# Kernel tuning notes

Measured on AMD Instinct MI355X. Metric: run time of the kernel, lower is better.

The kernel has to match this reference:

```python
import jax, jax.numpy as jnp
import numpy as np

N, E = 50000, 800000
IN_DIM, HID, OUT_DIM = 512, 64, 40


def setup_inputs() -> dict:
    key = jax.random.key(0)
    ks = jax.random.split(key, 7)
    X = jax.random.normal(ks[0], (N, IN_DIM), dtype=jnp.float32)
    edges = jax.random.randint(ks[1], (2, E), 0, N, dtype=jnp.int64)
    # GCNConv weight (glorot) and bias
    W1 = jax.random.normal(ks[2], (IN_DIM, HID), dtype=jnp.float32) / np.sqrt(IN_DIM)
    b1 = jnp.zeros((HID,), dtype=jnp.float32)
    # fc Linear
    Wfc = jax.random.normal(ks[3], (OUT_DIM, HID), dtype=jnp.float32) / np.sqrt(HID)
    bfc = jax.random.normal(ks[4], (OUT_DIM,), dtype=jnp.float32) * 0.01
    return {"X": X, "edges": edges, "W1": W1, "b1": b1, "Wfc": Wfc, "bfc": bfc}


def gcn_conv(x, src, dst, W, b, n):
    # PyG GCNConv: transform, add self-loops, symmetric D^-1/2 A D^-1/2 norm,
    # scatter-add messages at destination, add bias.
    h = x @ W  # [N, HID]
    loop = jnp.arange(n, dtype=src.dtype)
    src = jnp.concatenate([src, loop])
    dst = jnp.concatenate([dst, loop])
    deg = jax.ops.segment_sum(jnp.ones_like(dst, dtype=h.dtype), dst, num_segments=n)
    dinv = jnp.where(deg > 0, jax.lax.rsqrt(deg), 0.0)
    coef = dinv[src] * dinv[dst]  # [E+N]
    msgs = coef[:, None] * h[src]  # gather + scale
    agg = jax.ops.segment_sum(msgs, dst, num_segments=n)  # scatter-add
    return agg + b


def reference(X, edges, W1, b1, Wfc, bfc):
    n = X.shape[0]
    src, dst = edges[0], edges[1]
    h = jax.nn.relu(gcn_conv(X, src, dst, W1, b1, n))  # [N, HID]
    return h @ Wfc.T + bfc  # [N, OUT_DIM]
```

## Files before the change

kernel.cpp:

```cpp
#include <hip/hip_runtime.h>
#include <hip/hip_bf16.h>

typedef unsigned short u16;
typedef __bf16 bf16_8 __attribute__((ext_vector_type(8)));
typedef float f32_4 __attribute__((ext_vector_type(4)));

#define IN_DIM 512
#define HID 64
#define OUT_DIM 40
#define CAP 64
#define CF_GRID 2048

__global__ void k_prep(const float* __restrict__ W1, u16* __restrict__ W1t,
                       int* __restrict__ cnt, int n) {
    int i = blockIdx.x * 256 + threadIdx.x;
    if (i < n) cnt[i] = 0;
    if (i < IN_DIM * HID) {
        int k = i / HID, o = i % HID;
        __hip_bfloat16 v = __float2bfloat16(W1[i]);
        W1t[o * IN_DIM + k] = *reinterpret_cast<u16*>(&v);
    }
}

__launch_bounds__(256)
__global__ void k_cf(const int* __restrict__ src, const int* __restrict__ dst,
                     int* cnt, u16* __restrict__ csr, int E) {
    int e = blockIdx.x * 256 + threadIdx.x;
    const int stride = CF_GRID * 256;
    for (; e < E; e += stride) {
        int d = dst[e];
        int p = atomicAdd(&cnt[d], 1);
        if (p < CAP) csr[(size_t)d * CAP + p] = (u16)src[e];
    }
}

__launch_bounds__(512)
__global__ void k_gemm(const float* __restrict__ X, const u16* __restrict__ W1t,
                       u16* __restrict__ hs, int N) {
    __shared__ __align__(16) u16 As[2][2][64 * 40];
    __shared__ __align__(16) float Red[64 * 64];
    const int t = threadIdx.x;
    const int g = t >> 8;
    const int wl = (t >> 6) & 3;
    const int lane = t & 63;
    const int m = lane & 15;
    const int quad = lane >> 4;
    const int n0 = blockIdx.x * 64;

    f32_4 acc[4];
    #pragma unroll
    for (int c = 0; c < 4; c++) acc[c] = (f32_4){0.f, 0.f, 0.f, 0.f};

    const int tg = t & 255;
    const int r_st = tg >> 2;
    const int k_st = (tg & 3) * 8;

    int row = n0 + r_st; if (row >= N) row = N - 1;
    const float* xp = X + (size_t)row * IN_DIM + g * 256 + k_st;

    f32_4 x0 = *reinterpret_cast<const f32_4*>(xp);
    f32_4 x1 = *reinterpret_cast<const f32_4*>(xp + 4);

    int buf = 0;
    for (int ks = 0; ks < 256; ks += 32) {
        u16 xb[8];
        #pragma unroll
        for (int q = 0; q < 4; q++) {
            __hip_bfloat16 c0 = __float2bfloat16(x0[q]);
            __hip_bfloat16 c1 = __float2bfloat16(x1[q]);
            xb[q]     = *reinterpret_cast<u16*>(&c0);
            xb[4 + q] = *reinterpret_cast<u16*>(&c1);
        }
        *reinterpret_cast<uint4*>(&As[g][buf][r_st * 40 + k_st]) = *reinterpret_cast<uint4*>(xb);
        __syncthreads();

        if (ks + 32 < 256) {
            x0 = *reinterpret_cast<const f32_4*>(xp + ks + 32);
            x1 = *reinterpret_cast<const f32_4*>(xp + ks + 36);
        }

        bf16_8 a = *reinterpret_cast<const bf16_8*>(&As[g][buf][(wl * 16 + m) * 40 + quad * 8]);
        #pragma unroll
        for (int c = 0; c < 4; c++) {
            bf16_8 b = *reinterpret_cast<const bf16_8*>(
                W1t + (size_t)(c * 16 + m) * IN_DIM + g * 256 + ks + quad * 8);
            acc[c] = __builtin_amdgcn_mfma_f32_16x16x32_bf16(a, b, acc[c], 0, 0, 0);
        }
        buf ^= 1;
    }

    if (g == 1) {
        #pragma unroll
        for (int r = 0; r < 4; r++)
            #pragma unroll
            for (int c = 0; c < 4; c++)
                Red[(wl * 16 + quad * 4 + r) * 64 + c * 16 + m] = acc[c][r];
    }
    __syncthreads();
    if (g == 0) {
        const int nbase = n0 + wl * 16 + quad * 4;
        #pragma unroll
        for (int r = 0; r < 4; r++) {
            int n = nbase + r;
            if (n < N) {
                #pragma unroll
                for (int c = 0; c < 4; c++) {
                    float s = acc[c][r] + Red[(wl * 16 + quad * 4 + r) * 64 + c * 16 + m];
                    __hip_bfloat16 hv = __float2bfloat16(s);
                    hs[(size_t)n * HID + c * 16 + m] = *reinterpret_cast<u16*>(&hv);
                }
            }
        }
    }
}

__global__ void k_scale(u16* __restrict__ hs, const int* __restrict__ cnt, int N) {
    int i = blockIdx.x * 256 + threadIdx.x;
    int node = i >> 3;
    if (node >= N) return;
    float dv = rsqrtf((float)cnt[node] + 1.0f);
    uint4 v = *reinterpret_cast<uint4*>(hs + (size_t)i * 8);
    uint vv[4] = {v.x, v.y, v.z, v.w};
    u16 o[8];
    #pragma unroll
    for (int q = 0; q < 4; q++) {
        float lo = __uint_as_float(vv[q] << 16) * dv;
        float hi = __uint_as_float(vv[q] & 0xFFFF0000u) * dv;
        __hip_bfloat16 bl_ = __float2bfloat16(lo);
        __hip_bfloat16 bh_ = __float2bfloat16(hi);
        o[2 * q]     = *reinterpret_cast<u16*>(&bl_);
        o[2 * q + 1] = *reinterpret_cast<u16*>(&bh_);
    }
    *reinterpret_cast<uint4*>(hs + (size_t)i * 8) = *reinterpret_cast<uint4*>(o);
}

__device__ __forceinline__ void acc_add(f32_4& a, uint2 v) {
    a[0] += __uint_as_float(v.x << 16);
    a[1] += __uint_as_float(v.x & 0xFFFF0000u);
    a[2] += __uint_as_float(v.y << 16);
    a[3] += __uint_as_float(v.y & 0xFFFF0000u);
}

#define SHP 72

__launch_bounds__(256)
__global__ void k_aggfc(const u16* __restrict__ hs, const u16* __restrict__ csr,
                        const int* __restrict__ cnt, const float* __restrict__ b1,
                        const float* __restrict__ Wfc, const float* __restrict__ bfc,
                        float* __restrict__ out, int N) {
    __shared__ __align__(16) u16 shb[16 * SHP];
    __shared__ __align__(16) u16 wfb[48 * SHP];
    __shared__ float bl[48];
    const int t = threadIdx.x;

    for (int i = t; i < 48 * HID; i += 256) {
        int o = i / HID, k = i % HID;
        float v = (o < OUT_DIM) ? Wfc[o * HID + k] : 0.f;
        __hip_bfloat16 b = __float2bfloat16(v);
        wfb[o * SHP + k] = *reinterpret_cast<u16*>(&b);
    }
    if (t < 48) bl[t] = (t < OUT_DIM) ? bfc[t] : 0.f;

    const int g = t >> 4, l = t & 15;
    const int n = blockIdx.x * 16 + g;

    if (n < N) {
        const uint2* hs2 = reinterpret_cast<const uint2*>(hs);
        f32_4 aa[4];
        #pragma unroll
        for (int q = 0; q < 4; q++) aa[q] = (f32_4){0.f, 0.f, 0.f, 0.f};
        const float dvn = rsqrtf((float)cnt[n] + 1.0f);
        acc_add(aa[0], hs2[(size_t)n * 16 + l]);
        int deg = cnt[n]; if (deg > CAP) deg = CAP;
        uint2 cv = reinterpret_cast<const uint2*>(csr + (size_t)n * CAP)[l];
        const int nn1 = N - 1;
        for (int j = 0; j < deg; j += 16) {
            int base = j >> 2;
            uint wx[4], wy[4];
            #pragma unroll
            for (int q = 0; q < 4; q++) {
                wx[q] = __shfl(cv.x, base + q, 16);
                wy[q] = __shfl(cv.y, base + q, 16);
            }
            int s[16];
            #pragma unroll
            for (int q = 0; q < 4; q++) {
                s[4 * q + 0] = (int)(wx[q] & 0xffff);
                s[4 * q + 1] = (int)(wx[q] >> 16);
                s[4 * q + 2] = (int)(wy[q] & 0xffff);
                s[4 * q + 3] = (int)(wy[q] >> 16);
            }
            uint2 v[16];
            #pragma unroll
            for (int i = 0; i < 16; i++) {
                int si = s[i] < nn1 ? s[i] : nn1;
                v[i] = hs2[(size_t)si * 16 + l];
            }
            #pragma unroll
            for (int i = 0; i < 16; i++) {
                if (j + i >= deg) { v[i].x = 0u; v[i].y = 0u; }
                acc_add(aa[i & 3], v[i]);
            }
        }
        f32_4 acc = (aa[0] + aa[1]) + (aa[2] + aa[3]);
        u16 rb[4];
        #pragma unroll
        for (int q = 0; q < 4; q++) {
            float x = dvn * acc[q] + b1[l * 4 + q];
            x = x > 0.f ? x : 0.f;
            __hip_bfloat16 hb = __float2bfloat16(x);
            rb[q] = *reinterpret_cast<u16*>(&hb);
        }
        *reinterpret_cast<uint2*>(&shb[g * SHP + l * 4]) = *reinterpret_cast<uint2*>(rb);
    }
    __syncthreads();

    const int wave = t >> 6;
    const int lane = t & 63;
    const int m = lane & 15;
    const int quad = lane >> 4;
    if (wave < 3) {
        bf16_8 a0 = *reinterpret_cast<const bf16_8*>(&shb[m * SHP + quad * 8]);
        bf16_8 a1 = *reinterpret_cast<const bf16_8*>(&shb[m * SHP + 32 + quad * 8]);
        bf16_8 b0 = *reinterpret_cast<const bf16_8*>(&wfb[(wave * 16 + m) * SHP + quad * 8]);
        bf16_8 b1 = *reinterpret_cast<const bf16_8*>(&wfb[(wave * 16 + m) * SHP + 32 + quad * 8]);
        f32_4 c = (f32_4){0.f, 0.f, 0.f, 0.f};
        c = __builtin_amdgcn_mfma_f32_16x16x32_bf16(a0, b0, c, 0, 0, 0);
        c = __builtin_amdgcn_mfma_f32_16x16x32_bf16(a1, b1, c, 0, 0, 0);
        const int o = wave * 16 + m;
        if (o < OUT_DIM) {
            const int base = blockIdx.x * 16;
            #pragma unroll
            for (int r = 0; r < 4; r++) {
                int node = base + quad * 4 + r;
                if (node < N) out[(size_t)node * OUT_DIM + o] = c[r] + bl[o];
            }
        }
    }
}


extern "C" void kernel_launch(void* const* d_in, const int* in_sizes, int n_in,
                              void* d_out, int out_size, void* d_ws, size_t ws_size,
                              hipStream_t stream) {
    const float* X   = (const float*)d_in[0];
    const int* edges = (const int*)d_in[1];
    const float* W1  = (const float*)d_in[2];
    const float* b1  = (const float*)d_in[3];
    const float* Wfc = (const float*)d_in[4];
    const float* bfc = (const float*)d_in[5];

    const int N = in_sizes[0] / IN_DIM;
    const int E = in_sizes[1] / 2;
    const int* src = edges;
    const int* dst = edges + E;

    char* p = (char*)d_ws;
    auto carve = [&](size_t bytes) -> char* {
        char* r = p;
        p += (bytes + 255) & ~(size_t)255;
        return r;
    };
    u16* W1t = (u16*)carve((size_t)IN_DIM * HID * 2);
    u16* hs  = (u16*)carve((size_t)N * HID * 2);
    int* cnt = (int*)carve((size_t)N * 4);
    u16* csr = (u16*)carve((size_t)N * CAP * 2);

    const int nb = (N + 255) / 256;
    const int NT = (N + 63) / 64;

    k_prep <<<nb, 256, 0, stream>>>(W1, W1t, cnt, N);
    k_cf   <<<CF_GRID, 256, 0, stream>>>(src, dst, cnt, csr, E);
    k_gemm <<<NT, 512, 0, stream>>>(X, W1t, hs, N);
    k_scale<<<(N * 8 + 255) / 256, 256, 0, stream>>>(hs, cnt, N);
    k_aggfc<<<(N + 15) / 16, 256, 0, stream>>>(hs, csr, cnt, b1, Wfc, bfc,
                                               (float*)d_out, N);
}
```

Baseline: 259.2 us.

## Merge edge CSR build into GEMM kernel as extra blocks to overlap

```diff
diff --git a/kernel.cpp b/kernel.cpp
--- a/kernel.cpp
+++ b/kernel.cpp
@@ -9,7 +9,7 @@
 #define HID 64
 #define OUT_DIM 40
 #define CAP 64
-#define CF_GRID 2048
+#define CF_BLK 256
 
 __global__ void k_prep(const float* __restrict__ W1, u16* __restrict__ W1t,
                        int* __restrict__ cnt, int n) {
@@ -22,30 +22,40 @@
     }
 }
 
-__launch_bounds__(256)
-__global__ void k_cf(const int* __restrict__ src, const int* __restrict__ dst,
-                     int* cnt, u16* __restrict__ csr, int E) {
-    int e = blockIdx.x * 256 + threadIdx.x;
-    const int stride = CF_GRID * 256;
-    for (; e < E; e += stride) {
-        int d = dst[e];
-        int p = atomicAdd(&cnt[d], 1);
-        if (p < CAP) csr[(size_t)d * CAP + p] = (u16)src[e];
-    }
-}
-
 __launch_bounds__(512)
-__global__ void k_gemm(const float* __restrict__ X, const u16* __restrict__ W1t,
-                       u16* __restrict__ hs, int N) {
+__global__ void k_work(const float* __restrict__ X, const u16* __restrict__ W1t,
+                       const int* __restrict__ src, const int* __restrict__ dst,
+                       int* cnt, u16* __restrict__ csr, u16* __restrict__ hs,
+                       int N, int E) {
     __shared__ __align__(16) u16 As[2][2][64 * 40];
     __shared__ __align__(16) float Red[64 * 64];
     const int t = threadIdx.x;
+
+    if ((int)blockIdx.x < CF_BLK) {
+        int e = (int)blockIdx.x * 512 + t;
+        const int stride = CF_BLK * 512;
+        for (; e + stride < E; e += 2 * stride) {
+            int d0 = dst[e], d1 = dst[e + stride];
+            int s0 = src[e], s1 = src[e + stride];
+            int p0 = atomicAdd(&cnt[d0], 1);
+            int p1 = atomicAdd(&cnt[d1], 1);
+            if (p0 < CAP) csr[(size_t)d0 * CAP + p0] = (u16)s0;
+            if (p1 < CAP) csr[(size_t)d1 * CAP + p1] = (u16)s1;
+        }
+        for (; e < E; e += stride) {
+            int d = dst[e];
+            int p = atomicAdd(&cnt[d], 1);
+            if (p < CAP) csr[(size_t)d * CAP + p] = (u16)src[e];
+        }
+        return;
+    }
+
     const int g = t >> 8;
     const int wl = (t >> 6) & 3;
     const int lane = t & 63;
     const int m = lane & 15;
     const int quad = lane >> 4;
-    const int n0 = blockIdx.x * 64;
+    const int n0 = ((int)blockIdx.x - CF_BLK) * 64;
 
     f32_4 acc[4];
     #pragma unroll
@@ -270,8 +280,7 @@
     const int NT = (N + 63) / 64;
 
     k_prep <<<nb, 256, 0, stream>>>(W1, W1t, cnt, N);
-    k_cf   <<<CF_GRID, 256, 0, stream>>>(src, dst, cnt, csr, E);
-    k_gemm <<<NT, 512, 0, stream>>>(X, W1t, hs, N);
+    k_work <<<CF_BLK + NT, 512, 0, stream>>>(X, W1t, src, dst, cnt, csr, hs, N, E);
     k_scale<<<(N * 8 + 255) / 256, 256, 0, stream>>>(hs, cnt, N);
     k_aggfc<<<(N + 15) / 16, 256, 0, stream>>>(hs, csr, cnt, b1, Wfc, bfc,
                                                (float*)d_out, N);
```

New measurement: 241.2 us. -6.9%, faster.

## Partition edges by destination slice and overlap CSR build with GEMM

Applied to the files above, without the earlier changes.

```diff
diff --git a/kernel.cpp b/kernel.cpp
--- a/kernel.cpp
+++ b/kernel.cpp
@@ -2,6 +2,7 @@
 #include <hip/hip_bf16.h>
 
 typedef unsigned short u16;
+typedef unsigned int u32;
 typedef __bf16 bf16_8 __attribute__((ext_vector_type(8)));
 typedef float f32_4 __attribute__((ext_vector_type(4)));
 
@@ -9,12 +10,16 @@
 #define HID 64
 #define OUT_DIM 40
 #define CAP 64
-#define CF_GRID 2048
+#define DR_BLK 256
+#define PB 1024
+#define LCAP 224
+#define BCAP 132768
 
 __global__ void k_prep(const float* __restrict__ W1, u16* __restrict__ W1t,
-                       int* __restrict__ cnt, int n) {
+                       int* __restrict__ cnt, int* __restrict__ gtails, int n) {
     int i = blockIdx.x * 256 + threadIdx.x;
     if (i < n) cnt[i] = 0;
+    if (i < 8) gtails[i] = 0;
     if (i < IN_DIM * HID) {
         int k = i / HID, o = i % HID;
         __hip_bfloat16 v = __float2bfloat16(W1[i]);
@@ -23,29 +28,77 @@
 }
 
 __launch_bounds__(256)
-__global__ void k_cf(const int* __restrict__ src, const int* __restrict__ dst,
-                     int* cnt, u16* __restrict__ csr, int E) {
-    int e = blockIdx.x * 256 + threadIdx.x;
-    const int stride = CF_GRID * 256;
-    for (; e < E; e += stride) {
+__global__ void k_part(const int* __restrict__ src, const int* __restrict__ dst,
+                       u32* __restrict__ gbkt, int* __restrict__ gtails, int N, int E) {
+    __shared__ u32 lb[8][LCAP];
+    __shared__ int lcnt[8];
+    __shared__ int lbase[8];
+    const int t = threadIdx.x;
+    if (t < 8) lcnt[t] = 0;
+    __syncthreads();
+    const int per = (E + PB - 1) / PB;
+    const int e0 = (int)blockIdx.x * per;
+    int e1 = e0 + per; if (e1 > E) e1 = E;
+    for (int e = e0 + t; e < e1; e += 256) {
         int d = dst[e];
-        int p = atomicAdd(&cnt[d], 1);
-        if (p < CAP) csr[(size_t)d * CAP + p] = (u16)src[e];
+        int s = src[e];
+        int b = (int)((u32)(d * 8) / (u32)N);
+        int lo_b = (int)(((u32)b * (u32)N + 7) >> 3);
+        u32 entry = ((u32)(d - lo_b) << 16) | (u32)s;
+        int p = atomicAdd(&lcnt[b], 1);
+        if (p < LCAP) lb[b][p] = entry;
+        else {
+            int gi = atomicAdd(&gtails[b], 1);
+            if (gi < BCAP) gbkt[(size_t)b * BCAP + gi] = entry;
+        }
+    }
+    __syncthreads();
+    if (t < 8) {
+        int c = lcnt[t]; if (c > LCAP) c = LCAP;
+        lcnt[t] = c;
+        lbase[t] = atomicAdd(&gtails[t], c);
+    }
+    __syncthreads();
+    #pragma unroll 1
+    for (int b = 0; b < 8; b++) {
+        int c = lcnt[b], base = lbase[b];
+        for (int i = t; i < c; i += 256) {
+            int gi = base + i;
+            if (gi < BCAP) gbkt[(size_t)b * BCAP + gi] = lb[b][i];
+        }
     }
 }
 
 __launch_bounds__(512)
-__global__ void k_gemm(const float* __restrict__ X, const u16* __restrict__ W1t,
-                       u16* __restrict__ hs, int N) {
+__global__ void k_work(const float* __restrict__ X, const u16* __restrict__ W1t,
+                       const u32* __restrict__ gbkt, const int* __restrict__ gtails,
+                       int* cnt, u16* __restrict__ csr, u16* __restrict__ hs, int N) {
     __shared__ __align__(16) u16 As[2][2][64 * 40];
     __shared__ __align__(16) float Red[64 * 64];
     const int t = threadIdx.x;
+
+    if ((int)blockIdx.x < DR_BLK) {
+        const int slice = (int)blockIdx.x & 7;
+        const int rank  = (int)blockIdx.x >> 3;
+        const int lo_b  = (int)(((u32)slice * (u32)N + 7) >> 3);
+        int ce = gtails[slice]; if (ce > BCAP) ce = BCAP;
+        const u32* bp = gbkt + (size_t)slice * BCAP;
+        const int stride = (DR_BLK / 8) * 512;
+        for (int i = rank * 512 + t; i < ce; i += stride) {
+            u32 en = bp[i];
+            int d = lo_b + (int)(en >> 16);
+            int p = atomicAdd(&cnt[d], 1);
+            if (p < CAP) csr[(size_t)d * CAP + p] = (u16)(en & 0xffffu);
+        }
+        return;
+    }
+
     const int g = t >> 8;
     const int wl = (t >> 6) & 3;
     const int lane = t & 63;
     const int m = lane & 15;
     const int quad = lane >> 4;
-    const int n0 = blockIdx.x * 64;
+    const int n0 = ((int)blockIdx.x - DR_BLK) * 64;
 
     f32_4 acc[4];
     #pragma unroll
@@ -261,17 +314,19 @@
         p += (bytes + 255) & ~(size_t)255;
         return r;
     };
-    u16* W1t = (u16*)carve((size_t)IN_DIM * HID * 2);
-    u16* hs  = (u16*)carve((size_t)N * HID * 2);
-    int* cnt = (int*)carve((size_t)N * 4);
-    u16* csr = (u16*)carve((size_t)N * CAP * 2);
+    u16* W1t   = (u16*)carve((size_t)IN_DIM * HID * 2);
+    u16* hs    = (u16*)carve((size_t)N * HID * 2);
+    int* cnt   = (int*)carve((size_t)N * 4);
+    u16* csr   = (u16*)carve((size_t)N * CAP * 2);
+    int* gtails= (int*)carve(8 * 4);
+    u32* gbkt  = (u32*)carve((size_t)8 * BCAP * 4);
 
     const int nb = (N + 255) / 256;
     const int NT = (N + 63) / 64;
 
-    k_prep <<<nb, 256, 0, stream>>>(W1, W1t, cnt, N);
-    k_cf   <<<CF_GRID, 256, 0, stream>>>(src, dst, cnt, csr, E);
-    k_gemm <<<NT, 512, 0, stream>>>(X, W1t, hs, N);
+    k_prep <<<nb, 256, 0, stream>>>(W1, W1t, cnt, gtails, N);
+    k_part <<<PB, 256, 0, stream>>>(src, dst, gbkt, gtails, N, E);
+    k_work <<<DR_BLK + NT, 512, 0, stream>>>(X, W1t, gbkt, gtails, cnt, csr, hs, N);
     k_scale<<<(N * 8 + 255) / 256, 256, 0, stream>>>(hs, cnt, N);
     k_aggfc<<<(N + 15) / 16, 256, 0, stream>>>(hs, csr, cnt, b1, Wfc, bfc,
                                                (float*)d_out, N);
```

Result: faster. 247.9 us (-4.4%).
